# Optimization experiments

Hardware: AMD Instinct MI355X
Metric: run time of the kernel (lower is better)

## Reference

```python
import jax, jax.numpy as jnp
import numpy as np

B, N, F_IN, F_OUT, H, SE_DIM = 16, 1024, 64, 64, 4, 64
ALPHA = 0.2  # LeakyReLU negative slope


def setup_inputs() -> dict:
    key = jax.random.key(0)
    ks = jax.random.split(key, 8)
    x = jax.random.normal(ks[0], (B, N, F_IN), dtype=jnp.float32)
    adj = (jax.random.uniform(ks[1], (B, N, N)) < 0.05).astype(jnp.float32)
    SE = jax.random.normal(ks[2], (N, SE_DIM), dtype=jnp.float32)
    fin = F_IN + SE_DIM
    s_w = float(np.sqrt(2.0) * np.sqrt(6.0 / (fin + F_OUT)))
    s_a = float(np.sqrt(2.0) * np.sqrt(6.0 / (F_OUT + 1)))
    s_p = float(np.sqrt(2.0) * np.sqrt(6.0 / (H + H)))
    W = jax.random.uniform(ks[3], (H, fin, F_OUT), minval=-s_w, maxval=s_w, dtype=jnp.float32)
    a1 = jax.random.uniform(ks[4], (H, F_OUT), minval=-s_a, maxval=s_a, dtype=jnp.float32)
    a2 = jax.random.uniform(ks[5], (H, F_OUT), minval=-s_a, maxval=s_a, dtype=jnp.float32)
    P_l = jax.random.uniform(ks[6], (H, H), minval=-s_p, maxval=s_p, dtype=jnp.float32)
    P_w = jax.random.uniform(ks[7], (H, H), minval=-s_p, maxval=s_p, dtype=jnp.float32)
    return {"x": x, "adj": adj, "SE": SE, "W": W, "a1": a1, "a2": a2, "P_l": P_l, "P_w": P_w}


def reference(x, adj, SE, W, a1, a2, P_l, P_w):
    b, n, _ = x.shape
    # needSE: concat positional/structural embedding (repeated over batch)
    xi = jnp.concatenate([x, jnp.broadcast_to(SE[None], (b, n, SE.shape[-1]))], axis=2)
    # per-head projection: h[b,h,n,o]
    h = jnp.einsum('bnf,hfo->bhno', xi, W)
    f1 = jnp.einsum('bhno,ho->bhn', h, a1)
    f2 = jnp.einsum('bhno,ho->bhn', h, a2)
    # e[b,h,i,j] = leaky_relu(f1[i] + f2[j])
    e = jax.nn.leaky_relu(f1[:, :, :, None] + f2[:, :, None, :], negative_slope=ALPHA)
    # talking-heads mixing before softmax (P_l); softmax over the i (row/source) axis
    e = jnp.einsum('bhij,hg->bgij', e, P_l)
    att = jax.nn.softmax(e, axis=2)
    # talking-heads mixing after softmax (P_w)
    att = jnp.einsum('bgij,gh->bhij', att, P_w)
    # adjacency masking (dropout p=0 -> identity)
    att = att * adj[:, None]
    # aggregation + residual (in == out features, no downsample) + ELU
    out = jnp.einsum('bhij,bhjo->bhio', att, h)
    out = jax.nn.elu(out + x[:, None])
    bb, hh, nn_, oo = out.shape
    # concat heads along feature dim (head order preserved)
    return out.transpose(0, 2, 1, 3).reshape(bb, nn_, hh * oo)
```

## Files before the change

### kernel.cpp

```cpp
#include <hip/hip_runtime.h>
#include <hip/hip_bf16.h>

#define NB 16
#define NN 1024
#define FOUT 64
#define NH 4
#define LRELU_A 0.2f
#define CAP 192

typedef __attribute__((ext_vector_type(8))) short bf16x8;
typedef __attribute__((ext_vector_type(4))) float f32x4;

#define WFENCE() asm volatile("s_waitcnt lgkmcnt(0)" ::: "memory")

__device__ __forceinline__ float lrelu(float s) { return fmaxf(s, LRELU_A * s); }

__device__ __forceinline__ float4 min4(float4 a, float4 b) {
    return make_float4(fminf(a.x,b.x), fminf(a.y,b.y), fminf(a.z,b.z), fminf(a.w,b.w));
}
__device__ __forceinline__ float4 max4(float4 a, float4 b) {
    return make_float4(fmaxf(a.x,b.x), fmaxf(a.y,b.y), fmaxf(a.z,b.z), fmaxf(a.w,b.w));
}

__device__ __forceinline__ unsigned int pk2(float a, float b) {
    union { __hip_bfloat16 h; unsigned short u; } ua, ub;
    ua.h = __float2bfloat16(a); ub.h = __float2bfloat16(b);
    return (unsigned int)ua.u | ((unsigned int)ub.u << 16);
}
__device__ __forceinline__ unsigned short bfbits(float a) {
    union { __hip_bfloat16 h; unsigned short u; } ua;
    ua.h = __float2bfloat16(a);
    return ua.u;
}
__device__ __forceinline__ int toff(int r, int c) { return (r * 16 + (c ^ (r & 7))) * 16; }

__global__ __launch_bounds__(256) void k_proj(const float* __restrict__ x,
                                              const float* __restrict__ SE,
                                              const float* __restrict__ W,
                                              const float* __restrict__ a1,
                                              const float* __restrict__ a2,
                                              unsigned int* __restrict__ hbu,
                                              float* __restrict__ f1p,
                                              float* __restrict__ f2p)
{
    __shared__ char smem[49152];
    char* Ab = smem;
    char* Bb = smem + 32768;
    const int tid = threadIdx.x;
    const int rt  = blockIdx.x >> 2;
    const int ch  = blockIdx.x & 3;

    {
        const int row = tid & 127, kh = tid >> 7;
        const int rg = rt * 128 + row;
        const int bb = rg >> 10, nn = rg & 1023;
        const float4* src = (kh == 0) ? (const float4*)(x + ((size_t)(bb * NN + nn)) * 64)
                                      : (const float4*)(SE + (size_t)nn * 64);
        #pragma unroll
        for (int q = 0; q < 8; ++q) {
            float4 u0 = src[q * 2], u1 = src[q * 2 + 1];
            uint4 pkv = { pk2(u0.x, u0.y), pk2(u0.z, u0.w), pk2(u1.x, u1.y), pk2(u1.z, u1.w) };
            *(uint4*)(Ab + toff(row, kh * 8 + q)) = pkv;
        }
    }
    {
        const float* wbase = W + ch * 8192;
        #pragma unroll
        for (int q = 0; q < 4; ++q) {
            int gid = tid + 256 * q;
            int col = gid & 63, c = gid >> 6;
            const float* wp = wbase + (c * 8) * 64 + col;
            float v[8];
            #pragma unroll
            for (int j = 0; j < 8; ++j) v[j] = wp[j * 64];
            uint4 pkv = { pk2(v[0], v[1]), pk2(v[2], v[3]), pk2(v[4], v[5]), pk2(v[6], v[7]) };
            *(uint4*)(Bb + toff(col, c)) = pkv;
        }
    }
    __syncthreads();

    const int l = tid & 63, w = tid >> 6;
    const int r0 = 32 * w + (l & 15);
    const int ci = l >> 4;
    f32x4 acc[2][4];
    #pragma unroll
    for (int a = 0; a < 2; ++a)
        #pragma unroll
        for (int bf = 0; bf < 4; ++bf) { acc[a][bf][0]=0.f; acc[a][bf][1]=0.f; acc[a][bf][2]=0.f; acc[a][bf][3]=0.f; }

    #pragma unroll
    for (int ks = 0; ks < 4; ++ks) {
        const int c = 4 * ks + ci;
        bf16x8 A0 = *(const bf16x8*)(Ab + toff(r0,      c));
        bf16x8 A1 = *(const bf16x8*)(Ab + toff(r0 + 16, c));
        #pragma unroll
        for (int bf = 0; bf < 4; ++bf) {
            bf16x8 Bf = *(const bf16x8*)(Bb + toff(16 * bf + (l & 15), c));
            acc[0][bf] = __builtin_amdgcn_mfma_f32_16x16x32_bf16(A0, Bf, acc[0][bf], 0, 0, 0);
            acc[1][bf] = __builtin_amdgcn_mfma_f32_16x16x32_bf16(A1, Bf, acc[1][bf], 0, 0, 0);
        }
    }

    {
        float a1v[4], a2v[4];
        #pragma unroll
        for (int bf = 0; bf < 4; ++bf) {
            a1v[bf] = a1[ch * 64 + 16 * bf + (l & 15)];
            a2v[bf] = a2[ch * 64 + 16 * bf + (l & 15)];
        }
        #pragma unroll
        for (int a = 0; a < 2; ++a)
            #pragma unroll
            for (int reg = 0; reg < 4; ++reg) {
                float s1 = 0.f, s2 = 0.f;
                #pragma unroll
                for (int bf = 0; bf < 4; ++bf) {
                    s1 = fmaf(acc[a][bf][reg], a1v[bf], s1);
                    s2 = fmaf(acc[a][bf][reg], a2v[bf], s2);
                }
                #pragma unroll
                for (int m = 1; m < 16; m <<= 1) {
                    s1 += __shfl_xor(s1, m);
                    s2 += __shfl_xor(s2, m);
                }
                if ((l & 15) == 0) {
                    int r  = 16 * a + (l >> 4) * 4 + reg;
                    int ng = rt * 128 + 32 * w + r;
                    int bb = ng >> 10, n2 = ng & 1023;
                    f1p[(bb * NN + n2) * 4 + ch] = s1;
                    f2p[(bb * NN + n2) * 4 + ch] = s2;
                }
            }
    }
    __syncthreads();

    unsigned short* cst = (unsigned short*)smem + w * 2048;
    #pragma unroll
    for (int a = 0; a < 2; ++a)
        #pragma unroll
        for (int bf = 0; bf < 4; ++bf)
            #pragma unroll
            for (int reg = 0; reg < 4; ++reg) {
                int r   = 16 * a + (l >> 4) * 4 + reg;
                int col = 16 * bf + (l & 15);
                cst[r * 64 + col] = bfbits(acc[a][bf][reg]);
            }
    WFENCE();
    const uint4* csv = (const uint4*)cst;
    #pragma unroll
    for (int p = 0; p < 4; ++p) {
        int idx = p * 64 + l;
        uint4 v = csv[idx];
        int r = idx >> 3, o8 = idx & 7;
        int ng = rt * 128 + 32 * w + r;
        int bb = ng >> 10, n2 = ng & 1023;
        ((uint4*)hbu)[((size_t)(bb * NH + ch) * NN + n2) * 8 + o8] = v;
    }
}

__global__ __launch_bounds__(256) void k_stats(const float* __restrict__ f1p,
                                               const float* __restrict__ f2p,
                                               const float* __restrict__ P_l,
                                               float* __restrict__ Mp,
                                               float* __restrict__ Rp)
{
    __shared__ float4 f1s[1024];
    __shared__ float4 red[32][8];
    const int tid  = threadIdx.x;
    const int lane = tid & 63;
    const int b    = blockIdx.x >> 7;
    const int jt   = blockIdx.x & 127;
    const float4* f1p4 = (const float4*)f1p;
    const float4* f2p4 = (const float4*)f2p;

    #pragma unroll
    for (int q = 0; q < 4; ++q) f1s[tid + 256 * q] = f1p4[b * NN + tid + 256 * q];
    __syncthreads();

    float4 mn = make_float4( INFINITY,  INFINITY,  INFINITY,  INFINITY);
    float4 mx = make_float4(-INFINITY, -INFINITY, -INFINITY, -INFINITY);
    #pragma unroll
    for (int q = 0; q < 16; ++q) {
        float4 v = f1s[lane + 64 * q];
        mn = min4(mn, v);
        mx = max4(mx, v);
    }
    #pragma unroll
    for (int m = 32; m > 0; m >>= 1) {
        float4 on = make_float4(__shfl_xor(mn.x, m), __shfl_xor(mn.y, m), __shfl_xor(mn.z, m), __shfl_xor(mn.w, m));
        float4 ox = make_float4(__shfl_xor(mx.x, m), __shfl_xor(mx.y, m), __shfl_xor(mx.z, m), __shfl_xor(mx.w, m));
        mn = min4(mn, on);
        mx = max4(mx, ox);
    }

    float pl[4][4];
    #pragma unroll
    for (int hh = 0; hh < 4; ++hh)
        #pragma unroll
        for (int g = 0; g < 4; ++g) pl[hh][g] = P_l[hh * 4 + g];

    const int jj = tid & 7, ic = tid >> 3;
    const int j  = jt * 8 + jj;
    float4 f2v = f2p4[b * NN + j];
    float f2a[4] = {f2v.x, f2v.y, f2v.z, f2v.w};
    float mna[4] = {mn.x, mn.y, mn.z, mn.w};
    float mxa[4] = {mx.x, mx.y, mx.z, mx.w};
    float mub[4];
    #pragma unroll
    for (int g = 0; g < 4; ++g) {
        float s = 0.f;
        #pragma unroll
        for (int hh = 0; hh < 4; ++hh) {
            float base = (pl[hh][g] >= 0.f ? mxa[hh] : mna[hh]) + f2a[hh];
            s = fmaf(pl[hh][g], lrelu(base), s);
        }
        mub[g] = s;
    }

    float d[4] = {0.f, 0.f, 0.f, 0.f};
    #pragma unroll 4
    for (int ii = 0; ii < 32; ++ii) {
        int i = ic * 32 + ((ii + 2 * ic) & 31);
        float4 f1v = f1s[i];
        float l0 = lrelu(f1v.x + f2a[0]);
        float l1 = lrelu(f1v.y + f2a[1]);
        float l2 = lrelu(f1v.z + f2a[2]);
        float l3 = lrelu(f1v.w + f2a[3]);
        #pragma unroll
        for (int g = 0; g < 4; ++g) {
            float e = fmaf(pl[0][g], l0, fmaf(pl[1][g], l1, fmaf(pl[2][g], l2, pl[3][g] * l3)));
            d[g] += __expf(e - mub[g]);
        }
    }
    red[ic][jj] = make_float4(d[0], d[1], d[2], d[3]);
    __syncthreads();
    if (tid < 8) {
        float4 t = red[0][tid];
        #pragma unroll
        for (int r = 1; r < 32; ++r) {
            float4 u = red[r][tid];
            t.x += u.x; t.y += u.y; t.z += u.z; t.w += u.w;
        }
        ((float4*)Rp)[b * NN + j] = make_float4(1.f / t.x, 1.f / t.y, 1.f / t.z, 1.f / t.w);
        ((float4*)Mp)[b * NN + j] = make_float4(mub[0], mub[1], mub[2], mub[3]);
    }
}

__global__ __launch_bounds__(256) void k_agg(const float* __restrict__ adj,
                                             const float* __restrict__ x,
                                             const unsigned int* __restrict__ hb,
                                             const float* __restrict__ f1p,
                                             const float* __restrict__ f2p,
                                             const float* __restrict__ Mp,
                                             const float* __restrict__ Rp,
                                             const float* __restrict__ P_l,
                                             const float* __restrict__ P_w,
                                             float* __restrict__ out)
{
    __shared__ int   jl[4][CAP + 8];
    __shared__ float attlT[4][4][CAP + 8];
    const int tid  = threadIdx.x;
    const int w    = tid >> 6;
    const int lane = tid & 63;
    const int orig = blockIdx.x;
    const int swz  = (orig & 7) * 512 + (orig >> 3);
    const int row  = swz * 4 + w;
    const int b    = row >> 10;

    const float4* arow = (const float4*)adj + (size_t)row * 256;
    float4 av[4];
    #pragma unroll
    for (int q = 0; q < 4; ++q) av[q] = arow[lane + 64 * q];

    const unsigned long long lt = (1ull << lane) - 1ull;
    int cnt = 0;
    #pragma unroll
    for (int q = 0; q < 4; ++q) {
        float vv[4] = {av[q].x, av[q].y, av[q].z, av[q].w};
        #pragma unroll
        for (int c = 0; c < 4; ++c) {
            bool nz = (vv[c] != 0.f);
            unsigned long long mask = __ballot(nz);
            if (nz) {
                int pos = cnt + __popcll(mask & lt);
                if (pos < CAP) jl[w][pos] = (lane + 64 * q) * 4 + c;
            }
            cnt += __popcll(mask);
        }
    }
    if (cnt > CAP) cnt = CAP;
    if (lane < 8) jl[w][cnt + lane] = 0;
    WFENCE();

    float pl[4][4], pw[4][4];
    #pragma unroll
    for (int a_ = 0; a_ < 4; ++a_)
        #pragma unroll
        for (int g = 0; g < 4; ++g) {
            pl[a_][g] = P_l[a_ * 4 + g];
            pw[a_][g] = P_w[a_ * 4 + g];
        }
    const float4 f1v = ((const float4*)f1p)[row];
    for (int base = 0; base < cnt; base += 64) {
        int kk = base + lane;
        if (kk < cnt) {
            int j = jl[w][kk];
            float4 f2v = ((const float4*)f2p)[b * NN + j];
            float4 mv  = ((const float4*)Mp)[b * NN + j];
            float4 rv  = ((const float4*)Rp)[b * NN + j];
            float l0 = lrelu(f1v.x + f2v.x);
            float l1 = lrelu(f1v.y + f2v.y);
            float l2 = lrelu(f1v.z + f2v.z);
            float l3 = lrelu(f1v.w + f2v.w);
            float p0 = __expf(fmaf(pl[0][0], l0, fmaf(pl[1][0], l1, fmaf(pl[2][0], l2, pl[3][0] * l3))) - mv.x) * rv.x;
            float p1 = __expf(fmaf(pl[0][1], l0, fmaf(pl[1][1], l1, fmaf(pl[2][1], l2, pl[3][1] * l3))) - mv.y) * rv.y;
            float p2 = __expf(fmaf(pl[0][2], l0, fmaf(pl[1][2], l1, fmaf(pl[2][2], l2, pl[3][2] * l3))) - mv.z) * rv.z;
            float p3 = __expf(fmaf(pl[0][3], l0, fmaf(pl[1][3], l1, fmaf(pl[2][3], l2, pl[3][3] * l3))) - mv.w) * rv.w;
            #pragma unroll
            for (int g = 0; g < 4; ++g)
                attlT[w][g][kk] =
                    fmaf(p0, pw[0][g], fmaf(p1, pw[1][g], fmaf(p2, pw[2][g], p3 * pw[3][g])));
        }
    }
    if (lane < 8) {
        #pragma unroll
        for (int g = 0; g < 4; ++g) attlT[w][g][cnt + lane] = 0.f;
    }
    WFENCE();

    const int e2  = lane >> 5;
    const int sub = lane & 31;
    const int hh  = sub >> 3;
    const int oct = sub & 7;
    const uint4* hrow = (const uint4*)hb + ((size_t)(b * NH + hh) * NN) * 8 + oct;
    const float* atp = &attlT[w][hh][0];
    float acc[8];
    #pragma unroll
    for (int e = 0; e < 8; ++e) acc[e] = 0.f;

    #pragma unroll 2
    for (int base = 0; base < cnt; base += 8) {
        int j0 = jl[w][base     + e2];
        int j1 = jl[w][base + 2 + e2];
        int j2 = jl[w][base + 4 + e2];
        int j3 = jl[w][base + 6 + e2];
        uint4 u0 = hrow[(size_t)j0 * 8];
        uint4 u1 = hrow[(size_t)j1 * 8];
        uint4 u2 = hrow[(size_t)j2 * 8];
        uint4 u3 = hrow[(size_t)j3 * 8];
        float t0 = atp[base     + e2];
        float t1 = atp[base + 2 + e2];
        float t2 = atp[base + 4 + e2];
        float t3 = atp[base + 6 + e2];
        acc[0] = fmaf(t0, __uint_as_float(u0.x << 16),          acc[0]);
        acc[1] = fmaf(t0, __uint_as_float(u0.x & 0xffff0000u),  acc[1]);
        acc[2] = fmaf(t0, __uint_as_float(u0.y << 16),          acc[2]);
        acc[3] = fmaf(t0, __uint_as_float(u0.y & 0xffff0000u),  acc[3]);
        acc[4] = fmaf(t0, __uint_as_float(u0.z << 16),          acc[4]);
        acc[5] = fmaf(t0, __uint_as_float(u0.z & 0xffff0000u),  acc[5]);
        acc[6] = fmaf(t0, __uint_as_float(u0.w << 16),          acc[6]);
        acc[7] = fmaf(t0, __uint_as_float(u0.w & 0xffff0000u),  acc[7]);
        acc[0] = fmaf(t1, __uint_as_float(u1.x << 16),          acc[0]);
        acc[1] = fmaf(t1, __uint_as_float(u1.x & 0xffff0000u),  acc[1]);
        acc[2] = fmaf(t1, __uint_as_float(u1.y << 16),          acc[2]);
        acc[3] = fmaf(t1, __uint_as_float(u1.y & 0xffff0000u),  acc[3]);
        acc[4] = fmaf(t1, __uint_as_float(u1.z << 16),          acc[4]);
        acc[5] = fmaf(t1, __uint_as_float(u1.z & 0xffff0000u),  acc[5]);
        acc[6] = fmaf(t1, __uint_as_float(u1.w << 16),          acc[6]);
        acc[7] = fmaf(t1, __uint_as_float(u1.w & 0xffff0000u),  acc[7]);
        acc[0] = fmaf(t2, __uint_as_float(u2.x << 16),          acc[0]);
        acc[1] = fmaf(t2, __uint_as_float(u2.x & 0xffff0000u),  acc[1]);
        acc[2] = fmaf(t2, __uint_as_float(u2.y << 16),          acc[2]);
        acc[3] = fmaf(t2, __uint_as_float(u2.y & 0xffff0000u),  acc[3]);
        acc[4] = fmaf(t2, __uint_as_float(u2.z << 16),          acc[4]);
        acc[5] = fmaf(t2, __uint_as_float(u2.z & 0xffff0000u),  acc[5]);
        acc[6] = fmaf(t2, __uint_as_float(u2.w << 16),          acc[6]);
        acc[7] = fmaf(t2, __uint_as_float(u2.w & 0xffff0000u),  acc[7]);
        acc[0] = fmaf(t3, __uint_as_float(u3.x << 16),          acc[0]);
        acc[1] = fmaf(t3, __uint_as_float(u3.x & 0xffff0000u),  acc[1]);
        acc[2] = fmaf(t3, __uint_as_float(u3.y << 16),          acc[2]);
        acc[3] = fmaf(t3, __uint_as_float(u3.y & 0xffff0000u),  acc[3]);
        acc[4] = fmaf(t3, __uint_as_float(u3.z << 16),          acc[4]);
        acc[5] = fmaf(t3, __uint_as_float(u3.z & 0xffff0000u),  acc[5]);
        acc[6] = fmaf(t3, __uint_as_float(u3.w << 16),          acc[6]);
        acc[7] = fmaf(t3, __uint_as_float(u3.w & 0xffff0000u),  acc[7]);
    }

    #pragma unroll
    for (int e = 0; e < 8; ++e) acc[e] += __shfl_xor(acc[e], 32);

    if (e2 == 0) {
        const float4* x4 = (const float4*)x;
        float4 xa = x4[(size_t)row * 16 + oct * 2];
        float4 xb = x4[(size_t)row * 16 + oct * 2 + 1];
        float r0 = acc[0] + xa.x, r1 = acc[1] + xa.y, r2 = acc[2] + xa.z, r3 = acc[3] + xa.w;
        float r4 = acc[4] + xb.x, r5 = acc[5] + xb.y, r6 = acc[6] + xb.z, r7 = acc[7] + xb.w;
        float4 o4a, o4b;
        o4a.x = (r0 > 0.f) ? r0 : (__expf(r0) - 1.f);
        o4a.y = (r1 > 0.f) ? r1 : (__expf(r1) - 1.f);
        o4a.z = (r2 > 0.f) ? r2 : (__expf(r2) - 1.f);
        o4a.w = (r3 > 0.f) ? r3 : (__expf(r3) - 1.f);
        o4b.x = (r4 > 0.f) ? r4 : (__expf(r4) - 1.f);
        o4b.y = (r5 > 0.f) ? r5 : (__expf(r5) - 1.f);
        o4b.z = (r6 > 0.f) ? r6 : (__expf(r6) - 1.f);
        o4b.w = (r7 > 0.f) ? r7 : (__expf(r7) - 1.f);
        float4* op = (float4*)out + (size_t)row * 64 + hh * 16 + oct * 2;
        op[0] = o4a;
        op[1] = o4b;
    }
}

extern "C" void kernel_launch(void* const* d_in, const int* in_sizes, int n_in,
                              void* d_out, int out_size, void* d_ws, size_t ws_size,
                              hipStream_t stream)
{
    (void)in_sizes; (void)n_in; (void)out_size; (void)ws_size;
    const float* x   = (const float*)d_in[0];
    const float* adj = (const float*)d_in[1];
    const float* SE  = (const float*)d_in[2];
    const float* W   = (const float*)d_in[3];
    const float* a1  = (const float*)d_in[4];
    const float* a2  = (const float*)d_in[5];
    const float* P_l = (const float*)d_in[6];
    const float* P_w = (const float*)d_in[7];
    float* out = (float*)d_out;

    float* f1p = (float*)d_ws;
    float* f2p = f1p + 65536;
    float* Mp  = f2p + 65536;
    float* Rp  = Mp  + 65536;
    unsigned int* hbu = (unsigned int*)(Rp + 65536);

    k_proj <<<512,  256, 0, stream>>>(x, SE, W, a1, a2, hbu, f1p, f2p);
    k_stats<<<2048, 256, 0, stream>>>(f1p, f2p, P_l, Mp, Rp);
    k_agg  <<<4096, 256, 0, stream>>>(adj, x, hbu, f1p, f2p, Mp, Rp, P_l, P_w, out);
}
```

Measured before the change: 171.9 us.

## Process two rows per wave in aggregation and pack per-column softmax stats

The aggregation kernel now handles 8 rows per block, two per wave, so each half-wave owns one row and the cross-half shuffle reduction goes away. The gather loop reads four neighbor indices and attention weights with vector LDS loads. f2, max and reciprocal-sum are interleaved into a single SFT struct so each neighbor's stats need one contiguous fetch instead of three scattered ones. Adjacency reads and output writes use nontemporal hints, and CAP drops from 192 to 128, which risks truncating rows with many neighbors (at about 5% density the expected count is about 51).

```diff
diff --git a/kernel.cpp b/kernel.cpp
--- a/kernel.cpp
+++ b/kernel.cpp
@@ -6,12 +6,14 @@
 #define FOUT 64
 #define NH 4
 #define LRELU_A 0.2f
-#define CAP 192
+#define CAP 128
+#define RPB 8
 
 typedef __attribute__((ext_vector_type(8))) short bf16x8;
 typedef __attribute__((ext_vector_type(4))) float f32x4;
 
-#define WFENCE() asm volatile("s_waitcnt lgkmcnt(0)" ::: "memory")
+#define WFENCE() do { asm volatile("s_waitcnt lgkmcnt(0)" ::: "memory"); \
+                      __builtin_amdgcn_sched_barrier(0); } while (0)
 
 __device__ __forceinline__ float lrelu(float s) { return fmaxf(s, LRELU_A * s); }
 
@@ -161,8 +163,7 @@
 __global__ __launch_bounds__(256) void k_stats(const float* __restrict__ f1p,
                                                const float* __restrict__ f2p,
                                                const float* __restrict__ P_l,
-                                               float* __restrict__ Mp,
-                                               float* __restrict__ Rp)
+                                               float* __restrict__ SFT)
 {
     __shared__ float4 f1s[1024];
     __shared__ float4 red[32][8];
@@ -241,8 +242,10 @@
             float4 u = red[r][tid];
             t.x += u.x; t.y += u.y; t.z += u.z; t.w += u.w;
         }
-        ((float4*)Rp)[b * NN + j] = make_float4(1.f / t.x, 1.f / t.y, 1.f / t.z, 1.f / t.w);
-        ((float4*)Mp)[b * NN + j] = make_float4(mub[0], mub[1], mub[2], mub[3]);
+        float4* s4 = (float4*)SFT + ((size_t)(b * NN + j)) * 4;
+        s4[0] = f2v;
+        s4[1] = make_float4(mub[0], mub[1], mub[2], mub[3]);
+        s4[2] = make_float4(1.f / t.x, 1.f / t.y, 1.f / t.z, 1.f / t.w);
     }
 }
 
@@ -250,47 +253,20 @@
                                              const float* __restrict__ x,
                                              const unsigned int* __restrict__ hb,
                                              const float* __restrict__ f1p,
-                                             const float* __restrict__ f2p,
-                                             const float* __restrict__ Mp,
-                                             const float* __restrict__ Rp,
+                                             const float* __restrict__ SFT,
                                              const float* __restrict__ P_l,
                                              const float* __restrict__ P_w,
                                              float* __restrict__ out)
 {
-    __shared__ int   jl[4][CAP + 8];
-    __shared__ float attlT[4][4][CAP + 8];
+    __shared__ int   jl[RPB][CAP + 4];
+    __shared__ float attT[RPB][4][CAP + 4];
     const int tid  = threadIdx.x;
     const int w    = tid >> 6;
     const int lane = tid & 63;
     const int orig = blockIdx.x;
-    const int swz  = (orig & 7) * 512 + (orig >> 3);
-    const int row  = swz * 4 + w;
-    const int b    = row >> 10;
-
-    const float4* arow = (const float4*)adj + (size_t)row * 256;
-    float4 av[4];
-    #pragma unroll
-    for (int q = 0; q < 4; ++q) av[q] = arow[lane + 64 * q];
-
-    const unsigned long long lt = (1ull << lane) - 1ull;
-    int cnt = 0;
-    #pragma unroll
-    for (int q = 0; q < 4; ++q) {
-        float vv[4] = {av[q].x, av[q].y, av[q].z, av[q].w};
-        #pragma unroll
-        for (int c = 0; c < 4; ++c) {
-            bool nz = (vv[c] != 0.f);
-            unsigned long long mask = __ballot(nz);
-            if (nz) {
-                int pos = cnt + __popcll(mask & lt);
-                if (pos < CAP) jl[w][pos] = (lane + 64 * q) * 4 + c;
-            }
-            cnt += __popcll(mask);
-        }
-    }
-    if (cnt > CAP) cnt = CAP;
-    if (lane < 8) jl[w][cnt + lane] = 0;
-    WFENCE();
+    const int swz  = (orig & 7) * 256 + (orig >> 3);
+    const int rb   = swz * RPB;
+    const int b    = rb >> 10;
 
     float pl[4][4], pw[4][4];
     #pragma unroll
@@ -300,114 +276,147 @@
             pl[a_][g] = P_l[a_ * 4 + g];
             pw[a_][g] = P_w[a_ * 4 + g];
         }
-    const float4 f1v = ((const float4*)f1p)[row];
-    for (int base = 0; base < cnt; base += 64) {
-        int kk = base + lane;
-        if (kk < cnt) {
-            int j = jl[w][kk];
-            float4 f2v = ((const float4*)f2p)[b * NN + j];
-            float4 mv  = ((const float4*)Mp)[b * NN + j];
-            float4 rv  = ((const float4*)Rp)[b * NN + j];
-            float l0 = lrelu(f1v.x + f2v.x);
-            float l1 = lrelu(f1v.y + f2v.y);
-            float l2 = lrelu(f1v.z + f2v.z);
-            float l3 = lrelu(f1v.w + f2v.w);
-            float p0 = __expf(fmaf(pl[0][0], l0, fmaf(pl[1][0], l1, fmaf(pl[2][0], l2, pl[3][0] * l3))) - mv.x) * rv.x;
-            float p1 = __expf(fmaf(pl[0][1], l0, fmaf(pl[1][1], l1, fmaf(pl[2][1], l2, pl[3][1] * l3))) - mv.y) * rv.y;
-            float p2 = __expf(fmaf(pl[0][2], l0, fmaf(pl[1][2], l1, fmaf(pl[2][2], l2, pl[3][2] * l3))) - mv.z) * rv.z;
-            float p3 = __expf(fmaf(pl[0][3], l0, fmaf(pl[1][3], l1, fmaf(pl[2][3], l2, pl[3][3] * l3))) - mv.w) * rv.w;
+
+    const unsigned long long lt = (1ull << lane) - 1ull;
+    int cnts[2];
+    #pragma unroll
+    for (int s = 0; s < 2; ++s) {
+        const int slot = 2 * w + s;
+        const int row  = rb + slot;
+        const f32x4* arow = (const f32x4*)adj + (size_t)row * 256;
+        f32x4 av[4];
+        #pragma unroll
+        for (int q = 0; q < 4; ++q) av[q] = __builtin_nontemporal_load(arow + lane + 64 * q);
+        int cnt = 0;
+        #pragma unroll
+        for (int q = 0; q < 4; ++q) {
+            float vv[4] = {av[q][0], av[q][1], av[q][2], av[q][3]};
             #pragma unroll
-            for (int g = 0; g < 4; ++g)
-                attlT[w][g][kk] =
-                    fmaf(p0, pw[0][g], fmaf(p1, pw[1][g], fmaf(p2, pw[2][g], p3 * pw[3][g])));
-        }
-    }
-    if (lane < 8) {
-        #pragma unroll
-        for (int g = 0; g < 4; ++g) attlT[w][g][cnt + lane] = 0.f;
+            for (int c = 0; c < 4; ++c) {
+                bool nz = (vv[c] != 0.f);
+                unsigned long long mask = __ballot(nz);
+                if (nz) {
+                    int pos = cnt + __popcll(mask & lt);
+                    if (pos < CAP) jl[slot][pos] = (lane + 64 * q) * 4 + c;
+                }
+                cnt += __popcll(mask);
+            }
+        }
+        if (cnt > CAP) cnt = CAP;
+        if (lane < 4) jl[slot][cnt + lane] = 0;
+        cnts[s] = cnt;
     }
     WFENCE();
 
-    const int e2  = lane >> 5;
-    const int sub = lane & 31;
-    const int hh  = sub >> 3;
-    const int oct = sub & 7;
+    #pragma unroll
+    for (int s = 0; s < 2; ++s) {
+        const int slot = 2 * w + s;
+        const int row  = rb + slot;
+        const int cnt  = cnts[s];
+        const float4 f1v = ((const float4*)f1p)[row];
+        for (int base = 0; base < cnt; base += 64) {
+            int kk = base + lane;
+            if (kk < cnt) {
+                int j = jl[slot][kk];
+                const float4* s4 = (const float4*)SFT + ((size_t)(b * NN + j)) * 4;
+                float4 f2v = s4[0];
+                float4 mv  = s4[1];
+                float4 rv  = s4[2];
+                float l0 = lrelu(f1v.x + f2v.x);
+                float l1 = lrelu(f1v.y + f2v.y);
+                float l2 = lrelu(f1v.z + f2v.z);
+                float l3 = lrelu(f1v.w + f2v.w);
+                float p0 = __expf(fmaf(pl[0][0], l0, fmaf(pl[1][0], l1, fmaf(pl[2][0], l2, pl[3][0] * l3))) - mv.x) * rv.x;
+                float p1 = __expf(fmaf(pl[0][1], l0, fmaf(pl[1][1], l1, fmaf(pl[2][1], l2, pl[3][1] * l3))) - mv.y) * rv.y;
+                float p2 = __expf(fmaf(pl[0][2], l0, fmaf(pl[1][2], l1, fmaf(pl[2][2], l2, pl[3][2] * l3))) - mv.z) * rv.z;
+                float p3 = __expf(fmaf(pl[0][3], l0, fmaf(pl[1][3], l1, fmaf(pl[2][3], l2, pl[3][3] * l3))) - mv.w) * rv.w;
+                #pragma unroll
+                for (int g = 0; g < 4; ++g)
+                    attT[slot][g][kk] =
+                        fmaf(p0, pw[0][g], fmaf(p1, pw[1][g], fmaf(p2, pw[2][g], p3 * pw[3][g])));
+            }
+        }
+        if (lane < 4) {
+            #pragma unroll
+            for (int g = 0; g < 4; ++g) attT[slot][g][cnts[s] + lane] = 0.f;
+        }
+    }
+    WFENCE();
+
+    const int hw   = lane >> 5;
+    const int sub  = lane & 31;
+    const int hh   = sub >> 3;
+    const int oct  = sub & 7;
+    const int slot = 2 * w + hw;
+    const int row  = rb + slot;
+    const int cnt  = cnts[hw];
     const uint4* hrow = (const uint4*)hb + ((size_t)(b * NH + hh) * NN) * 8 + oct;
-    const float* atp = &attlT[w][hh][0];
+    const float* atp  = &attT[slot][hh][0];
+    const int*   jlp  = &jl[slot][0];
     float acc[8];
     #pragma unroll
     for (int e = 0; e < 8; ++e) acc[e] = 0.f;
 
-    #pragma unroll 2
-    for (int base = 0; base < cnt; base += 8) {
-        int j0 = jl[w][base     + e2];
-        int j1 = jl[w][base + 2 + e2];
-        int j2 = jl[w][base + 4 + e2];
-        int j3 = jl[w][base + 6 + e2];
-        uint4 u0 = hrow[(size_t)j0 * 8];
-        uint4 u1 = hrow[(size_t)j1 * 8];
-        uint4 u2 = hrow[(size_t)j2 * 8];
-        uint4 u3 = hrow[(size_t)j3 * 8];
-        float t0 = atp[base     + e2];
-        float t1 = atp[base + 2 + e2];
-        float t2 = atp[base + 4 + e2];
-        float t3 = atp[base + 6 + e2];
-        acc[0] = fmaf(t0, __uint_as_float(u0.x << 16),          acc[0]);
-        acc[1] = fmaf(t0, __uint_as_float(u0.x & 0xffff0000u),  acc[1]);
-        acc[2] = fmaf(t0, __uint_as_float(u0.y << 16),          acc[2]);
-        acc[3] = fmaf(t0, __uint_as_float(u0.y & 0xffff0000u),  acc[3]);
-        acc[4] = fmaf(t0, __uint_as_float(u0.z << 16),          acc[4]);
-        acc[5] = fmaf(t0, __uint_as_float(u0.z & 0xffff0000u),  acc[5]);
-        acc[6] = fmaf(t0, __uint_as_float(u0.w << 16),          acc[6]);
-        acc[7] = fmaf(t0, __uint_as_float(u0.w & 0xffff0000u),  acc[7]);
-        acc[0] = fmaf(t1, __uint_as_float(u1.x << 16),          acc[0]);
-        acc[1] = fmaf(t1, __uint_as_float(u1.x & 0xffff0000u),  acc[1]);
-        acc[2] = fmaf(t1, __uint_as_float(u1.y << 16),          acc[2]);
-        acc[3] = fmaf(t1, __uint_as_float(u1.y & 0xffff0000u),  acc[3]);
-        acc[4] = fmaf(t1, __uint_as_float(u1.z << 16),          acc[4]);
-        acc[5] = fmaf(t1, __uint_as_float(u1.z & 0xffff0000u),  acc[5]);
-        acc[6] = fmaf(t1, __uint_as_float(u1.w << 16),          acc[6]);
-        acc[7] = fmaf(t1, __uint_as_float(u1.w & 0xffff0000u),  acc[7]);
-        acc[0] = fmaf(t2, __uint_as_float(u2.x << 16),          acc[0]);
-        acc[1] = fmaf(t2, __uint_as_float(u2.x & 0xffff0000u),  acc[1]);
-        acc[2] = fmaf(t2, __uint_as_float(u2.y << 16),          acc[2]);
-        acc[3] = fmaf(t2, __uint_as_float(u2.y & 0xffff0000u),  acc[3]);
-        acc[4] = fmaf(t2, __uint_as_float(u2.z << 16),          acc[4]);
-        acc[5] = fmaf(t2, __uint_as_float(u2.z & 0xffff0000u),  acc[5]);
-        acc[6] = fmaf(t2, __uint_as_float(u2.w << 16),          acc[6]);
-        acc[7] = fmaf(t2, __uint_as_float(u2.w & 0xffff0000u),  acc[7]);
-        acc[0] = fmaf(t3, __uint_as_float(u3.x << 16),          acc[0]);
-        acc[1] = fmaf(t3, __uint_as_float(u3.x & 0xffff0000u),  acc[1]);
-        acc[2] = fmaf(t3, __uint_as_float(u3.y << 16),          acc[2]);
-        acc[3] = fmaf(t3, __uint_as_float(u3.y & 0xffff0000u),  acc[3]);
-        acc[4] = fmaf(t3, __uint_as_float(u3.z << 16),          acc[4]);
-        acc[5] = fmaf(t3, __uint_as_float(u3.z & 0xffff0000u),  acc[5]);
-        acc[6] = fmaf(t3, __uint_as_float(u3.w << 16),          acc[6]);
-        acc[7] = fmaf(t3, __uint_as_float(u3.w & 0xffff0000u),  acc[7]);
-    }
-
-    #pragma unroll
-    for (int e = 0; e < 8; ++e) acc[e] += __shfl_xor(acc[e], 32);
-
-    if (e2 == 0) {
-        const float4* x4 = (const float4*)x;
-        float4 xa = x4[(size_t)row * 16 + oct * 2];
-        float4 xb = x4[(size_t)row * 16 + oct * 2 + 1];
-        float r0 = acc[0] + xa.x, r1 = acc[1] + xa.y, r2 = acc[2] + xa.z, r3 = acc[3] + xa.w;
-        float r4 = acc[4] + xb.x, r5 = acc[5] + xb.y, r6 = acc[6] + xb.z, r7 = acc[7] + xb.w;
-        float4 o4a, o4b;
-        o4a.x = (r0 > 0.f) ? r0 : (__expf(r0) - 1.f);
-        o4a.y = (r1 > 0.f) ? r1 : (__expf(r1) - 1.f);
-        o4a.z = (r2 > 0.f) ? r2 : (__expf(r2) - 1.f);
-        o4a.w = (r3 > 0.f) ? r3 : (__expf(r3) - 1.f);
-        o4b.x = (r4 > 0.f) ? r4 : (__expf(r4) - 1.f);
-        o4b.y = (r5 > 0.f) ? r5 : (__expf(r5) - 1.f);
-        o4b.z = (r6 > 0.f) ? r6 : (__expf(r6) - 1.f);
-        o4b.w = (r7 > 0.f) ? r7 : (__expf(r7) - 1.f);
-        float4* op = (float4*)out + (size_t)row * 64 + hh * 16 + oct * 2;
-        op[0] = o4a;
-        op[1] = o4b;
-    }
+    #pragma unroll 1
+    for (int base = 0; base < cnt; base += 4) {
+        const int4   ja = *(const int4*)&jlp[base];
+        const float4 ta = *(const float4*)&atp[base];
+        uint4 u0 = hrow[(size_t)ja.x * 8];
+        uint4 u1 = hrow[(size_t)ja.y * 8];
+        uint4 u2 = hrow[(size_t)ja.z * 8];
+        uint4 u3 = hrow[(size_t)ja.w * 8];
+        acc[0] = fmaf(ta.x, __uint_as_float(u0.x << 16),          acc[0]);
+        acc[1] = fmaf(ta.x, __uint_as_float(u0.x & 0xffff0000u),  acc[1]);
+        acc[2] = fmaf(ta.x, __uint_as_float(u0.y << 16),          acc[2]);
+        acc[3] = fmaf(ta.x, __uint_as_float(u0.y & 0xffff0000u),  acc[3]);
+        acc[4] = fmaf(ta.x, __uint_as_float(u0.z << 16),          acc[4]);
+        acc[5] = fmaf(ta.x, __uint_as_float(u0.z & 0xffff0000u),  acc[5]);
+        acc[6] = fmaf(ta.x, __uint_as_float(u0.w << 16),          acc[6]);
+        acc[7] = fmaf(ta.x, __uint_as_float(u0.w & 0xffff0000u),  acc[7]);
+        acc[0] = fmaf(ta.y, __uint_as_float(u1.x << 16),          acc[0]);
+        acc[1] = fmaf(ta.y, __uint_as_float(u1.x & 0xffff0000u),  acc[1]);
+        acc[2] = fmaf(ta.y, __uint_as_float(u1.y << 16),          acc[2]);
+        acc[3] = fmaf(ta.y, __uint_as_float(u1.y & 0xffff0000u),  acc[3]);
+        acc[4] = fmaf(ta.y, __uint_as_float(u1.z << 16),          acc[4]);
+        acc[5] = fmaf(ta.y, __uint_as_float(u1.z & 0xffff0000u),  acc[5]);
+        acc[6] = fmaf(ta.y, __uint_as_float(u1.w << 16),          acc[6]);
+        acc[7] = fmaf(ta.y, __uint_as_float(u1.w & 0xffff0000u),  acc[7]);
+        acc[0] = fmaf(ta.z, __uint_as_float(u2.x << 16),          acc[0]);
+        acc[1] = fmaf(ta.z, __uint_as_float(u2.x & 0xffff0000u),  acc[1]);
+        acc[2] = fmaf(ta.z, __uint_as_float(u2.y << 16),          acc[2]);
+        acc[3] = fmaf(ta.z, __uint_as_float(u2.y & 0xffff0000u),  acc[3]);
+        acc[4] = fmaf(ta.z, __uint_as_float(u2.z << 16),          acc[4]);
+        acc[5] = fmaf(ta.z, __uint_as_float(u2.z & 0xffff0000u),  acc[5]);
+        acc[6] = fmaf(ta.z, __uint_as_float(u2.w << 16),          acc[6]);
+        acc[7] = fmaf(ta.z, __uint_as_float(u2.w & 0xffff0000u),  acc[7]);
+        acc[0] = fmaf(ta.w, __uint_as_float(u3.x << 16),          acc[0]);
+        acc[1] = fmaf(ta.w, __uint_as_float(u3.x & 0xffff0000u),  acc[1]);
+        acc[2] = fmaf(ta.w, __uint_as_float(u3.y << 16),          acc[2]);
+        acc[3] = fmaf(ta.w, __uint_as_float(u3.y & 0xffff0000u),  acc[3]);
+        acc[4] = fmaf(ta.w, __uint_as_float(u3.z << 16),          acc[4]);
+        acc[5] = fmaf(ta.w, __uint_as_float(u3.z & 0xffff0000u),  acc[5]);
+        acc[6] = fmaf(ta.w, __uint_as_float(u3.w << 16),          acc[6]);
+        acc[7] = fmaf(ta.w, __uint_as_float(u3.w & 0xffff0000u),  acc[7]);
+    }
+
+    const float4* x4 = (const float4*)x;
+    float4 xa = x4[(size_t)row * 16 + oct * 2];
+    float4 xb = x4[(size_t)row * 16 + oct * 2 + 1];
+    float r0 = acc[0] + xa.x, r1 = acc[1] + xa.y, r2 = acc[2] + xa.z, r3 = acc[3] + xa.w;
+    float r4 = acc[4] + xb.x, r5 = acc[5] + xb.y, r6 = acc[6] + xb.z, r7 = acc[7] + xb.w;
+    f32x4 o4a, o4b;
+    o4a[0] = (r0 > 0.f) ? r0 : (__expf(r0) - 1.f);
+    o4a[1] = (r1 > 0.f) ? r1 : (__expf(r1) - 1.f);
+    o4a[2] = (r2 > 0.f) ? r2 : (__expf(r2) - 1.f);
+    o4a[3] = (r3 > 0.f) ? r3 : (__expf(r3) - 1.f);
+    o4b[0] = (r4 > 0.f) ? r4 : (__expf(r4) - 1.f);
+    o4b[1] = (r5 > 0.f) ? r5 : (__expf(r5) - 1.f);
+    o4b[2] = (r6 > 0.f) ? r6 : (__expf(r6) - 1.f);
+    o4b[3] = (r7 > 0.f) ? r7 : (__expf(r7) - 1.f);
+    f32x4* op = (f32x4*)out + (size_t)row * 16 + hh * 4 + oct;
+    op = (f32x4*)out + (size_t)row * 64 + hh * 16 + oct * 2;
+    __builtin_nontemporal_store(o4a, op);
+    __builtin_nontemporal_store(o4b, op + 1);
 }
 
 extern "C" void kernel_launch(void* const* d_in, const int* in_sizes, int n_in,
@@ -427,11 +436,10 @@
 
     float* f1p = (float*)d_ws;
     float* f2p = f1p + 65536;
-    float* Mp  = f2p + 65536;
-    float* Rp  = Mp  + 65536;
-    unsigned int* hbu = (unsigned int*)(Rp + 65536);
+    float* SFT = f2p + 65536;
+    unsigned int* hbu = (unsigned int*)(SFT + 262144);
 
     k_proj <<<512,  256, 0, stream>>>(x, SE, W, a1, a2, hbu, f1p, f2p);
-    k_stats<<<2048, 256, 0, stream>>>(f1p, f2p, P_l, Mp, Rp);
-    k_agg  <<<4096, 256, 0, stream>>>(adj, x, hbu, f1p, f2p, Mp, Rp, P_l, P_w, out);
-}
+    k_stats<<<2048, 256, 0, stream>>>(f1p, f2p, P_l, SFT);
+    k_agg  <<<2048, 256, 0, stream>>>(adj, x, hbu, f1p, SFT, P_l, P_w, out);
+}
```

Result: slower. 177.7 us (+3.4%).
